# Optimization experiments

Measured on AMD Instinct MI355X. Metric: run time of the kernel, lower is better.

The kernel has to match this reference:

```python
import jax, jax.numpy as jnp
import numpy as np

N, E, G = 40000, 640000, 64
D_IN, D_EMB, D_HID, D_OUT = 128, 128, 128, 36


def setup_inputs() -> dict:
    key = jax.random.key(0)
    ks = jax.random.split(key, 12)
    x = jax.random.normal(ks[0], (N, D_IN), dtype=jnp.float32)
    edge_weight = jax.random.uniform(ks[1], (E,), dtype=jnp.float32)
    rho = jax.random.uniform(ks[2], (G,), dtype=jnp.float32)
    edge_index = jax.random.randint(ks[3], (2, E), 0, N, dtype=jnp.int32)
    batch = jnp.sort(jax.random.randint(ks[4], (N,), 0, G, dtype=jnp.int32))
    def lin(k, fi, fo):
        s = 1.0 / np.sqrt(fi)
        return jax.random.normal(k, (fi, fo), dtype=jnp.float32) * s
    conv_w = lin(ks[5], D_IN, D_EMB)
    conv_b = jnp.zeros((D_EMB,), jnp.float32)
    w1 = lin(ks[6], 2 * D_EMB + 1, D_HID); b1 = jnp.zeros((D_HID,), jnp.float32)
    w2 = lin(ks[7], D_HID, D_HID);        b2 = jnp.zeros((D_HID,), jnp.float32)
    w3 = lin(ks[8], D_HID, D_OUT);        b3 = jnp.zeros((D_OUT,), jnp.float32)
    return dict(x=x, edge_weight=edge_weight, rho=rho, conv_w=conv_w, conv_b=conv_b,
                w1=w1, b1=b1, w2=w2, b2=b2, w3=w3, b3=b3,
                edge_index=edge_index, batch=batch)


def _gcn_conv(h, edge_index, ew, W, b):
    # PyG GCNConv: add self-loops (weight 1), symmetric deg^-1/2 normalization,
    # linear transform, gather-scale-scatter aggregation, bias.
    n = h.shape[0]
    loop = jnp.arange(n, dtype=edge_index.dtype)
    src = jnp.concatenate([edge_index[0], loop])
    dst = jnp.concatenate([edge_index[1], loop])
    w_all = jnp.concatenate([ew, jnp.ones((n,), ew.dtype)])
    deg = jax.ops.segment_sum(w_all, dst, num_segments=n)
    dinv = jnp.where(deg > 0, jax.lax.rsqrt(deg), 0.0)
    norm = dinv[src] * w_all * dinv[dst]          # [E+N]
    hW = h @ W                                    # [N, D_EMB]
    msg = hW[src] * norm[:, None]                 # [E+N, D_EMB]
    return jax.ops.segment_sum(msg, dst, num_segments=n) + b


def reference(x, edge_weight, rho, conv_w, conv_b, w1, b1, w2, b2, w3, b3,
              edge_index, batch):
    h = jax.nn.relu(_gcn_conv(x, edge_index, edge_weight, conv_w, conv_b))
    g = G
    cnt = jax.ops.segment_sum(jnp.ones((h.shape[0],), h.dtype), batch, num_segments=g)
    hmax = jax.ops.segment_max(h, batch, num_segments=g)
    hmax = jnp.where(cnt[:, None] > 0, hmax, 0.0)
    hsum = jax.ops.segment_sum(h, batch, num_segments=g)
    hmean = hsum / jnp.maximum(cnt, 1.0)[:, None]
    hg = jnp.concatenate([hmax, hmean, rho[:, None]], axis=1)  # [G, 2*D_EMB+1]
    z = jax.nn.relu(hg @ w1 + b1)
    z = jax.nn.relu(z @ w2 + b2)
    return z @ w3 + b3
```

## Files before the change

kernel.cpp:

```cpp
#include <hip/hip_runtime.h>
#include <hip/hip_fp16.h>

static __device__ __forceinline__ float relu_f(float v) { return v > 0.f ? v : 0.f; }

typedef _Float16 half8 __attribute__((ext_vector_type(8)));
typedef float floatx4 __attribute__((ext_vector_type(4)));

#define ELL 96

static __device__ __forceinline__ float entry_w(unsigned int pk) {
  return __half2float(__ushort_as_half((unsigned short)(pk >> 16)));
}


__global__ __launch_bounds__(256) void count_fill_kernel(
    const int* __restrict__ src, const int* __restrict__ dst,
    const float* __restrict__ ew, unsigned long long* __restrict__ cnt,
    unsigned int* __restrict__ epack, int E,
    const float* __restrict__ W, _Float16* __restrict__ wt,
    const float* __restrict__ w1, float* __restrict__ w1t,
    const float* __restrict__ w2, float* __restrict__ w2t,
    const float* __restrict__ w3, float* __restrict__ w3t) {
  int i = blockIdx.x * blockDim.x + threadIdx.x;
  if (i < 16384) {
    int k = i >> 7, c = i & 127;
    wt[c * 128 + k] = (_Float16)W[i];
  } else if (i < 16384 + 32896) {
    int j = i - 16384;
    int k = j >> 7, c = j & 127;
    w1t[c * 260 + k] = w1[j];
  } else if (i < 16384 + 32896 + 16384) {
    int j = i - (16384 + 32896);
    int k = j >> 7, c = j & 127;
    w2t[c * 128 + k] = w2[j];
  } else if (i < 16384 + 32896 + 16384 + 4608) {
    int j = i - (16384 + 32896 + 16384);
    int k = j / 36, c = j - k * 36;
    w3t[c * 128 + k] = w3[j];
  }
  if (i >= E) return;
  int s = src[i];
  int d = dst[i];
  float w = ew[i];
  unsigned long long pk = (1ull << 32) |
      (unsigned long long)__float2uint_rn(w * 16777216.f);
  unsigned long long old = atomicAdd(&cnt[d], pk);
  unsigned int r = (unsigned int)(old >> 32);
  if (r < ELL) {
    unsigned short w16 = __half_as_ushort(__float2half_rn(w));
    epack[(size_t)d * ELL + r] = (unsigned int)s | ((unsigned int)w16 << 16);
  }
}


__global__ void premul_cast_kernel(const float4* __restrict__ x4,
                                   const unsigned long long* __restrict__ cnt,
                                   half8* __restrict__ xh8, int n) {
  int j = blockIdx.x * blockDim.x + threadIdx.x;
  if (j >= n * 16) return;
  int node = j >> 4;
  unsigned long long cv = cnt[node];
  float deg = 1.f + (float)(unsigned int)cv * (1.f / 16777216.f);
  float dinv = rsqrtf(deg);
  float4 a = x4[2 * j], b = x4[2 * j + 1];
  half8 o;
  o[0] = (_Float16)(a.x * dinv); o[1] = (_Float16)(a.y * dinv);
  o[2] = (_Float16)(a.z * dinv); o[3] = (_Float16)(a.w * dinv);
  o[4] = (_Float16)(b.x * dinv); o[5] = (_Float16)(b.y * dinv);
  o[6] = (_Float16)(b.z * dinv); o[7] = (_Float16)(b.w * dinv);
  xh8[j] = o;
}


__global__ __launch_bounds__(256) void agg_kernel(const half8* __restrict__ xh8,
    const unsigned long long* __restrict__ cnt,
    const unsigned int* __restrict__ epack,
    half8* __restrict__ hagg, int n) {
  int tid = threadIdx.x;
  int node = blockIdx.x * 16 + (tid >> 4);
  int sub = tid & 15;
  if (node >= n) return;
  unsigned long long cv = cnt[node];
  int deg = (int)(unsigned int)(cv >> 32);
  if (deg > ELL) deg = ELL;
  float dn = rsqrtf(1.f + (float)(unsigned int)cv * (1.f / 16777216.f));
  half8 xv = xh8[(size_t)node * 16 + sub];
  float acc[8];
  #pragma unroll
  for (int c = 0; c < 8; ++c) acc[c] = dn * (float)xv[c];
  size_t base = (size_t)node * ELL;
  int dlen = (deg + 7) & ~7;
  uint4 pa, pb;
  if (dlen > 0) {
    pa = *(const uint4*)&epack[base];
    pb = *(const uint4*)&epack[base + 4];
  }
  for (int j = 0; j < dlen; j += 8) {
    size_t nxt = (j + 8 < dlen) ? base + j + 8 : base;
    uint4 na = *(const uint4*)&epack[nxt];
    uint4 nb2 = *(const uint4*)&epack[nxt + 4];
    unsigned int pk[8] = {pa.x, pa.y, pa.z, pa.w, pb.x, pb.y, pb.z, pb.w};
    half8 hx[8];
    #pragma unroll
    for (int u = 0; u < 8; ++u) {
      int sidx = (j + u < deg) ? (int)(pk[u] & 0xFFFFu) : node;
      hx[u] = xh8[(size_t)sidx * 16 + sub];
    }
    #pragma unroll
    for (int u = 0; u < 8; ++u) {
      float wgt = (j + u < deg) ? entry_w(pk[u]) * dn : 0.f;
      #pragma unroll
      for (int c = 0; c < 8; ++c) acc[c] += wgt * (float)hx[u][c];
    }
    pa = na; pb = nb2;
  }
  half8 outv;
  #pragma unroll
  for (int c = 0; c < 8; ++c) outv[c] = (_Float16)acc[c];
  hagg[(size_t)node * 16 + sub] = outv;
}


__global__ __launch_bounds__(256) void gemm_pool_kernel(const half8* __restrict__ hagg,
    const _Float16* __restrict__ wt, const float* __restrict__ bias,
    const int* __restrict__ batch,
    float* __restrict__ gmax, float* __restrict__ gsum, float* __restrict__ gcnt, int n) {
  __shared__ float sH[64 * 129];
  __shared__ int sBatch[64];
  int tid = threadIdx.x;
  int w = tid >> 6, lane = tid & 63;
  int quad = lane >> 4, c15 = lane & 15;
  int row0 = blockIdx.x * 64;
  int nb = n - row0; if (nb > 64) nb = 64;

  int node = row0 + w * 16 + c15;
  if (node >= n) node = n - 1;
  half8 af[4];
  #pragma unroll
  for (int ks = 0; ks < 4; ++ks)
    af[ks] = hagg[(size_t)node * 16 + ks * 4 + quad];
  if (tid < nb) sBatch[tid] = batch[row0 + tid];

  float bb[8];
  #pragma unroll
  for (int j = 0; j < 8; ++j) bb[j] = bias[j * 16 + c15];

  floatx4 acc[8] = {};
  #pragma unroll
  for (int ks = 0; ks < 4; ++ks) {
    #pragma unroll
    for (int j = 0; j < 8; ++j) {
      const half8* bptr =
          (const half8*)(wt + (size_t)(j * 16 + c15) * 128 + ks * 32 + quad * 8);
      acc[j] = __builtin_amdgcn_mfma_f32_16x16x32_f16(af[ks], *bptr, acc[j], 0, 0, 0);
    }
  }

  #pragma unroll
  for (int j = 0; j < 8; ++j) {
    int col = j * 16 + c15;
    #pragma unroll
    for (int r = 0; r < 4; ++r) {
      int row = w * 16 + quad * 4 + r;
      if (row < nb) sH[row * 129 + col] = relu_f(acc[j][r] + bb[j]);
    }
  }
  __syncthreads();

  if (tid < 128) {
    int c = tid;
    int cur = sBatch[0];
    float mx = 0.f, sm = 0.f;
    int cnt_ = 0;
    for (int r = 0; r < nb; ++r) {
      int g = sBatch[r];
      if (g != cur) {
        atomicMax((int*)&gmax[cur * 128 + c], __float_as_int(mx));
        atomicAdd(&gsum[cur * 128 + c], sm);
        if (c == 0) atomicAdd(&gcnt[cur], (float)cnt_);
        mx = 0.f; sm = 0.f; cnt_ = 0; cur = g;
      }
      float v = sH[r * 129 + c];
      mx = fmaxf(mx, v);
      sm += v;
      ++cnt_;
    }
    atomicMax((int*)&gmax[cur * 128 + c], __float_as_int(mx));
    atomicAdd(&gsum[cur * 128 + c], sm);
    if (c == 0) atomicAdd(&gcnt[cur], (float)cnt_);
  }
}


__global__ __launch_bounds__(256) void mlp_kernel(const float* __restrict__ gmax,
    const float* __restrict__ gsum, const float* __restrict__ gcnt,
    const float* __restrict__ rho,
    const float* __restrict__ w1t, const float* __restrict__ b1,
    const float* __restrict__ w2t, const float* __restrict__ b2,
    const float* __restrict__ w3t, const float* __restrict__ b3,
    float* __restrict__ out) {
  __shared__ float s_in[260];
  __shared__ float s_part[256];
  __shared__ float s_z1[128];
  __shared__ float s_z2[128];
  int g = blockIdx.x, t = threadIdx.x;
  int col = t & 127, seg = t >> 7;
  float inv_cnt = 1.f / fmaxf(gcnt[g], 1.f);
  if (t < 128) s_in[t] = gmax[g * 128 + t];
  else         s_in[t] = gsum[g * 128 + col] * inv_cnt;
  if (t == 0)  s_in[256] = rho[g];
  __syncthreads();

  float s;
  {
    const float4* wp = (const float4*)(w1t + (size_t)col * 260 + seg * 128);
    const float4* sp = (const float4*)(s_in + seg * 128);
    float a = 0.f, b = 0.f;
    #pragma unroll
    for (int q = 0; q < 32; q += 2) {
      float4 u0 = wp[q],     i0 = sp[q];
      float4 u1 = wp[q + 1], i1 = sp[q + 1];
      a += u0.x * i0.x + u0.y * i0.y + u0.z * i0.z + u0.w * i0.w;
      b += u1.x * i1.x + u1.y * i1.y + u1.z * i1.z + u1.w * i1.w;
    }
    s = a + b;
    s += seg ? s_in[256] * w1t[(size_t)col * 260 + 256] : b1[col];
  }
  s_part[t] = s;
  __syncthreads();
  if (t < 128) s_z1[t] = relu_f(s_part[t] + s_part[t + 128]);
  __syncthreads();

  {
    const float4* wp = (const float4*)(w2t + (size_t)col * 128 + seg * 64);
    const float4* sp = (const float4*)(s_z1 + seg * 64);
    float a = 0.f, b = 0.f;
    #pragma unroll
    for (int q = 0; q < 16; q += 2) {
      float4 u0 = wp[q],     i0 = sp[q];
      float4 u1 = wp[q + 1], i1 = sp[q + 1];
      a += u0.x * i0.x + u0.y * i0.y + u0.z * i0.z + u0.w * i0.w;
      b += u1.x * i1.x + u1.y * i1.y + u1.z * i1.z + u1.w * i1.w;
    }
    s = a + b + (seg ? 0.f : b2[col]);
  }
  s_part[t] = s;
  __syncthreads();
  if (t < 128) s_z2[t] = relu_f(s_part[t] + s_part[t + 128]);
  __syncthreads();

  if (t < 144) {
    int oc = t % 36, sg = t / 36;
    const float4* wp = (const float4*)(w3t + (size_t)oc * 128 + sg * 32);
    const float4* sp = (const float4*)(s_z2 + sg * 32);
    float a = 0.f;
    #pragma unroll
    for (int q = 0; q < 8; ++q) {
      float4 u = wp[q], iv = sp[q];
      a += u.x * iv.x + u.y * iv.y + u.z * iv.z + u.w * iv.w;
    }
    s_part[t] = a;
  }
  __syncthreads();
  if (t < 36)
    out[g * 36 + t] = b3[t] + s_part[t] + s_part[t + 36] + s_part[t + 72] + s_part[t + 108];
}


extern "C" void kernel_launch(void* const* d_in, const int* in_sizes, int n_in,
                              void* d_out, int out_size, void* d_ws, size_t ws_size,
                              hipStream_t stream) {
  const float* x      = (const float*)d_in[0];
  const float* ew     = (const float*)d_in[1];
  const float* rho    = (const float*)d_in[2];
  const float* conv_w = (const float*)d_in[3];
  const float* conv_b = (const float*)d_in[4];
  const float* w1 = (const float*)d_in[5];
  const float* b1 = (const float*)d_in[6];
  const float* w2 = (const float*)d_in[7];
  const float* b2 = (const float*)d_in[8];
  const float* w3 = (const float*)d_in[9];
  const float* b3 = (const float*)d_in[10];
  const int* eidx  = (const int*)d_in[11];
  const int* batch = (const int*)d_in[12];

  const int N = in_sizes[0] / 128;
  const int E = in_sizes[1];
  const int G = in_sizes[2];
  const int* srcp = eidx;
  const int* dstp = eidx + E;

  char* p = (char*)d_ws;
  auto carve = [&](size_t bytes) { char* r = p; p += (bytes + 255) & ~(size_t)255; return (void*)r; };
  char* zbase = p;
  unsigned long long* cnt  = (unsigned long long*)carve((size_t)N * 8);
  float*              gmax = (float*)             carve((size_t)G * 128 * 4);
  float*              gsum = (float*)             carve((size_t)G * 128 * 4);
  float*              gcnt = (float*)             carve((size_t)G * 4);
  size_t zbytes = (size_t)(p - zbase);
  unsigned int* epack = (unsigned int*)carve((size_t)N * ELL * 4);
  half8*        xh    = (half8*)       carve((size_t)N * 128 * 2);
  half8*        hagg  = (half8*)       carve((size_t)N * 128 * 2);
  _Float16*     wt    = (_Float16*)    carve((size_t)128 * 128 * 2);
  float*        w1t   = (float*)       carve((size_t)128 * 260 * 4);
  float*        w2t   = (float*)       carve((size_t)128 * 128 * 4);
  float*        w3t   = (float*)       carve((size_t)36 * 128 * 4);

  hipMemsetAsync(zbase, 0, zbytes, stream);

  int nthr_cf = E;
  if (nthr_cf < 70272) nthr_cf = 70272;
  count_fill_kernel<<<(nthr_cf + 255) / 256, 256, 0, stream>>>(srcp, dstp, ew, cnt,
                                                               epack, E, conv_w, wt,
                                                               w1, w1t, w2, w2t, w3, w3t);
  premul_cast_kernel<<<(N * 16 + 255) / 256, 256, 0, stream>>>((const float4*)x, cnt, xh, N);
  agg_kernel<<<(N + 15) / 16, 256, 0, stream>>>(xh, cnt, epack, hagg, N);
  gemm_pool_kernel<<<(N + 63) / 64, 256, 0, stream>>>(hagg, wt, conv_b, batch,
                                                      gmax, gsum, gcnt, N);
  mlp_kernel<<<G, 256, 0, stream>>>(gmax, gsum, gcnt, rho, w1t, b1, w2t, b2, w3t, b3,
                                    (float*)d_out);
}
```

Measured before the change: 178.6 us.

## Fuse neighbor aggregation into GEMM+pool kernel and pad degree counters

Merges the sparse aggregation kernel into the MFMA GEMM/pooling kernel. Each block now aggregates its 64 nodes into shared memory and feeds the GEMM from there, which removes the hagg global round trip and one launch. It also spreads the per-node atomic counters over a 16-element stride to reduce atomic contention on shared cache lines, at the cost of a much larger memset. The fused kernel has fewer blocks (N/64 instead of N/16) and more register pressure, so latency hiding in the gather phase may suffer.

```diff
diff --git a/kernel.cpp b/kernel.cpp
--- a/kernel.cpp
+++ b/kernel.cpp
@@ -7,6 +7,7 @@
 typedef float floatx4 __attribute__((ext_vector_type(4)));
 
 #define ELL 96
+#define CNT_STRIDE 16
 
 static __device__ __forceinline__ float entry_w(unsigned int pk) {
   return __half2float(__ushort_as_half((unsigned short)(pk >> 16)));
@@ -44,7 +45,7 @@
   float w = ew[i];
   unsigned long long pk = (1ull << 32) |
       (unsigned long long)__float2uint_rn(w * 16777216.f);
-  unsigned long long old = atomicAdd(&cnt[d], pk);
+  unsigned long long old = atomicAdd(&cnt[(size_t)d * CNT_STRIDE], pk);
   unsigned int r = (unsigned int)(old >> 32);
   if (r < ELL) {
     unsigned short w16 = __half_as_ushort(__float2half_rn(w));
@@ -59,7 +60,7 @@
   int j = blockIdx.x * blockDim.x + threadIdx.x;
   if (j >= n * 16) return;
   int node = j >> 4;
-  unsigned long long cv = cnt[node];
+  unsigned long long cv = cnt[(size_t)node * CNT_STRIDE];
   float deg = 1.f + (float)(unsigned int)cv * (1.f / 16777216.f);
   float dinv = rsqrtf(deg);
   float4 a = x4[2 * j], b = x4[2 * j + 1];
@@ -72,74 +73,73 @@
 }
 
 
-__global__ __launch_bounds__(256) void agg_kernel(const half8* __restrict__ xh8,
+__global__ __launch_bounds__(256) void agg_gemm_pool_kernel(const half8* __restrict__ xh8,
     const unsigned long long* __restrict__ cnt,
-    const unsigned int* __restrict__ epack,
-    half8* __restrict__ hagg, int n) {
-  int tid = threadIdx.x;
-  int node = blockIdx.x * 16 + (tid >> 4);
-  int sub = tid & 15;
-  if (node >= n) return;
-  unsigned long long cv = cnt[node];
-  int deg = (int)(unsigned int)(cv >> 32);
-  if (deg > ELL) deg = ELL;
-  float dn = rsqrtf(1.f + (float)(unsigned int)cv * (1.f / 16777216.f));
-  half8 xv = xh8[(size_t)node * 16 + sub];
-  float acc[8];
-  #pragma unroll
-  for (int c = 0; c < 8; ++c) acc[c] = dn * (float)xv[c];
-  size_t base = (size_t)node * ELL;
-  int dlen = (deg + 7) & ~7;
-  uint4 pa, pb;
-  if (dlen > 0) {
-    pa = *(const uint4*)&epack[base];
-    pb = *(const uint4*)&epack[base + 4];
-  }
-  for (int j = 0; j < dlen; j += 8) {
-    size_t nxt = (j + 8 < dlen) ? base + j + 8 : base;
-    uint4 na = *(const uint4*)&epack[nxt];
-    uint4 nb2 = *(const uint4*)&epack[nxt + 4];
-    unsigned int pk[8] = {pa.x, pa.y, pa.z, pa.w, pb.x, pb.y, pb.z, pb.w};
-    half8 hx[8];
-    #pragma unroll
-    for (int u = 0; u < 8; ++u) {
-      int sidx = (j + u < deg) ? (int)(pk[u] & 0xFFFFu) : node;
-      hx[u] = xh8[(size_t)sidx * 16 + sub];
-    }
-    #pragma unroll
-    for (int u = 0; u < 8; ++u) {
-      float wgt = (j + u < deg) ? entry_w(pk[u]) * dn : 0.f;
-      #pragma unroll
-      for (int c = 0; c < 8; ++c) acc[c] += wgt * (float)hx[u][c];
-    }
-    pa = na; pb = nb2;
-  }
-  half8 outv;
-  #pragma unroll
-  for (int c = 0; c < 8; ++c) outv[c] = (_Float16)acc[c];
-  hagg[(size_t)node * 16 + sub] = outv;
-}
-
-
-__global__ __launch_bounds__(256) void gemm_pool_kernel(const half8* __restrict__ hagg,
-    const _Float16* __restrict__ wt, const float* __restrict__ bias,
-    const int* __restrict__ batch,
+    const unsigned int* __restrict__ epack, const _Float16* __restrict__ wt,
+    const float* __restrict__ bias, const int* __restrict__ batch,
     float* __restrict__ gmax, float* __restrict__ gsum, float* __restrict__ gcnt, int n) {
   __shared__ float sH[64 * 129];
+  _Float16* sAgg = (_Float16*)sH;
   __shared__ int sBatch[64];
   int tid = threadIdx.x;
   int w = tid >> 6, lane = tid & 63;
+  int grp = lane >> 4, sub = lane & 15;
   int quad = lane >> 4, c15 = lane & 15;
   int row0 = blockIdx.x * 64;
   int nb = n - row0; if (nb > 64) nb = 64;
 
-  int node = row0 + w * 16 + c15;
-  if (node >= n) node = n - 1;
+  #pragma unroll
+  for (int it = 0; it < 4; ++it) {
+    int rloc = w * 16 + it * 4 + grp;
+    int node = row0 + rloc;
+    if (node >= n) node = n - 1;
+    unsigned long long cv = cnt[(size_t)node * CNT_STRIDE];
+    int deg = (int)(unsigned int)(cv >> 32);
+    if (deg > ELL) deg = ELL;
+    float dn = rsqrtf(1.f + (float)(unsigned int)cv * (1.f / 16777216.f));
+    half8 xv = xh8[(size_t)node * 16 + sub];
+    float acc[8];
+    #pragma unroll
+    for (int c = 0; c < 8; ++c) acc[c] = dn * (float)xv[c];
+    size_t base = (size_t)node * ELL;
+    int dlen = (deg + 7) & ~7;
+    uint4 pa, pb;
+    if (dlen > 0) {
+      pa = *(const uint4*)&epack[base];
+      pb = *(const uint4*)&epack[base + 4];
+    }
+    for (int j = 0; j < dlen; j += 8) {
+      size_t nxt = (j + 8 < dlen) ? base + j + 8 : base;
+      uint4 na = *(const uint4*)&epack[nxt];
+      uint4 nb2 = *(const uint4*)&epack[nxt + 4];
+      unsigned int pk[8] = {pa.x, pa.y, pa.z, pa.w, pb.x, pb.y, pb.z, pb.w};
+      half8 hx[8];
+      #pragma unroll
+      for (int u = 0; u < 8; ++u) {
+        int sidx = (j + u < deg) ? (int)(pk[u] & 0xFFFFu) : node;
+        hx[u] = xh8[(size_t)sidx * 16 + sub];
+      }
+      #pragma unroll
+      for (int u = 0; u < 8; ++u) {
+        float wgt = (j + u < deg) ? entry_w(pk[u]) * dn : 0.f;
+        #pragma unroll
+        for (int c = 0; c < 8; ++c) acc[c] += wgt * (float)hx[u][c];
+      }
+      pa = na; pb = nb2;
+    }
+    half8 outv;
+    #pragma unroll
+    for (int c = 0; c < 8; ++c) outv[c] = (_Float16)acc[c];
+    *(half8*)&sAgg[rloc * 136 + sub * 8] = outv;
+  }
+  __syncthreads();
+
   half8 af[4];
   #pragma unroll
   for (int ks = 0; ks < 4; ++ks)
-    af[ks] = hagg[(size_t)node * 16 + ks * 4 + quad];
+    af[ks] = *(const half8*)&sAgg[(w * 16 + c15) * 136 + ks * 32 + quad * 8];
   if (tid < nb) sBatch[tid] = batch[row0 + tid];
+  __syncthreads();
 
   float bb[8];
   #pragma unroll
@@ -293,14 +293,13 @@
   char* p = (char*)d_ws;
   auto carve = [&](size_t bytes) { char* r = p; p += (bytes + 255) & ~(size_t)255; return (void*)r; };
   char* zbase = p;
-  unsigned long long* cnt  = (unsigned long long*)carve((size_t)N * 8);
+  unsigned long long* cnt  = (unsigned long long*)carve((size_t)N * CNT_STRIDE * 8);
   float*              gmax = (float*)             carve((size_t)G * 128 * 4);
   float*              gsum = (float*)             carve((size_t)G * 128 * 4);
   float*              gcnt = (float*)             carve((size_t)G * 4);
   size_t zbytes = (size_t)(p - zbase);
   unsigned int* epack = (unsigned int*)carve((size_t)N * ELL * 4);
   half8*        xh    = (half8*)       carve((size_t)N * 128 * 2);
-  half8*        hagg  = (half8*)       carve((size_t)N * 128 * 2);
   _Float16*     wt    = (_Float16*)    carve((size_t)128 * 128 * 2);
   float*        w1t   = (float*)       carve((size_t)128 * 260 * 4);
   float*        w2t   = (float*)       carve((size_t)128 * 128 * 4);
@@ -314,9 +313,8 @@
                                                                epack, E, conv_w, wt,
                                                                w1, w1t, w2, w2t, w3, w3t);
   premul_cast_kernel<<<(N * 16 + 255) / 256, 256, 0, stream>>>((const float4*)x, cnt, xh, N);
-  agg_kernel<<<(N + 15) / 16, 256, 0, stream>>>(xh, cnt, epack, hagg, N);
-  gemm_pool_kernel<<<(N + 63) / 64, 256, 0, stream>>>(hagg, wt, conv_b, batch,
-                                                      gmax, gsum, gcnt, N);
+  agg_gemm_pool_kernel<<<(N + 63) / 64, 256, 0, stream>>>(xh, cnt, epack, wt, conv_b,
+                                                          batch, gmax, gsum, gcnt, N);
   mlp_kernel<<<G, 256, 0, stream>>>(gmax, gsum, gcnt, rho, w1t, b1, w2t, b2, w3t, b3,
                                     (float*)d_out);
 }
```

Result: no change. 175.8 us (-1.5%).
